# Kernel optimization log

Measured on AMD Instinct MI355X. Metric: run time of the kernel, lower is better.

The kernel has to match this reference:

```python
import jax, jax.numpy as jnp
import numpy as np

DIM = 256
NUM_HEADS = 8
HEAD_DIM = DIM // NUM_HEADS
SCALE = HEAD_DIM ** -0.5


def setup_inputs() -> dict:
    key = jax.random.key(0)
    ks = jax.random.split(key, 8)
    B, C, H, W = 2, DIM, 64, 64
    s = 0.02
    return {
        "dec_feat": jax.random.normal(ks[0], (B, C, H, W), dtype=jnp.float32),
        "enc_feat": jax.random.normal(ks[1], (B, C, H, W), dtype=jnp.float32),
        "Wq": jax.random.normal(ks[2], (C, C), dtype=jnp.float32) * s,
        "bq": jnp.zeros((C,), dtype=jnp.float32),
        "Wkv": jax.random.normal(ks[3], (2 * C, C), dtype=jnp.float32) * s,
        "bkv": jnp.zeros((2 * C,), dtype=jnp.float32),
        "Wo": jax.random.normal(ks[4], (C, C), dtype=jnp.float32) * s,
        "bo": jnp.zeros((C,), dtype=jnp.float32),
    }


def reference(dec_feat, enc_feat, Wq, bq, Wkv, bkv, Wo, bo):
    B, C, H, W = dec_feat.shape
    N = H * W
    hd = HEAD_DIM
    # 1x1 convs == per-pixel linear maps over channels
    q = jnp.einsum('bchw,dc->bdhw', dec_feat, Wq) + bq[None, :, None, None]
    kv = jnp.einsum('bchw,dc->bdhw', enc_feat, Wkv) + bkv[None, :, None, None]
    k, v = jnp.split(kv, 2, axis=1)
    # [B, C, H, W] -> [B, heads, N, head_dim]
    def to_heads(x):
        return x.reshape(B, NUM_HEADS, hd, N).transpose(0, 1, 3, 2)
    qh, kh, vh = to_heads(q), to_heads(k), to_heads(v)
    attn = jnp.einsum('bhnd,bhmd->bhnm', qh, kh) * SCALE  # [B,h,N,N]
    attn = jax.nn.softmax(attn, axis=-1)
    out = jnp.einsum('bhnm,bhmd->bhnd', attn, vh)  # [B,h,N,hd]
    out = out.transpose(0, 1, 3, 2).reshape(B, C, H, W)
    out = jnp.einsum('bchw,dc->bdhw', out, Wo) + bo[None, :, None, None]
    return out
```

## Files before the change

kernel.cpp:

```cpp
#include <hip/hip_runtime.h>
#include <hip/hip_bf16.h>

#define B_ 2
#define C_ 256
#define N_ 4096
#define NH_ 8
#define HD_ 32
#define SCALE_ 0.17677669529663687f
#define LOG2E_ 1.4426950408889634f

typedef __attribute__((ext_vector_type(8))) short bf16x8;
typedef __attribute__((ext_vector_type(4))) float f32x4;

__device__ inline short f2b(float f) {
    __hip_bfloat16 h = __float2bfloat16(f);
    return __builtin_bit_cast(short, h);
}

__device__ inline unsigned pk2(float a, float b) {
    unsigned r;
    asm("v_cvt_pk_bf16_f32 %0, %1, %2" : "=v"(r) : "v"(a), "v"(b));
    return r;
}

__global__ __launch_bounds__(256) void wcvt(
    const float* __restrict__ Wq, const float* __restrict__ Wkv,
    const float* __restrict__ Wo, short* __restrict__ Wall)
{
    const int i = (blockIdx.x * 256 + threadIdx.x) * 8;
    const float* src; int off;
    if (i < 65536)       { src = Wq;  off = i; }
    else if (i < 196608) { src = Wkv; off = i - 65536; }
    else                 { src = Wo;  off = i - 196608; }
    float4 a = ((const float4*)(src + off))[0];
    float4 c = ((const float4*)(src + off))[1];
    uint2 u0, u1;
    u0.x = pk2(a.x, a.y); u0.y = pk2(a.z, a.w);
    u1.x = pk2(c.x, c.y); u1.y = pk2(c.z, c.w);
    *(uint2*)(Wall + i)     = u0;
    *(uint2*)(Wall + i + 4) = u1;
}

__global__ __launch_bounds__(256) void proj_qkv(
    const float* __restrict__ dec, const float* __restrict__ enc,
    const short* __restrict__ Wall, const float* __restrict__ bq,
    const float* __restrict__ bkv,
    short* __restrict__ Qb, short* __restrict__ Kb, short* __restrict__ Vb)
{
    const int b = blockIdx.z, y = blockIdx.y;
    const int n0 = blockIdx.x * 64;
    const float* In   = (y == 0) ? dec : enc;
    const float* bias = (y == 0) ? bq : ((y == 1) ? bkv : bkv + 256);
    const int wbase = y * 256;

    const int tid = threadIdx.x;
    const int w = tid >> 6, l = tid & 63, lg = l >> 4, lr = l & 15;

    __shared__ short eld[8][64][40];

    f32x4 acc[4][4] = {};
    const float* Inb = In + (size_t)b * C_ * N_;

    for (int c0 = 0; c0 < C_; c0 += 32) {
        bf16x8 af[4];
        #pragma unroll
        for (int db = 0; db < 4; db++)
            af[db] = *(const bf16x8*)&Wall[
                (size_t)(wbase + w * 64 + db * 16 + lr) * C_ + c0 + lg * 8];
        #pragma unroll
        for (int nb = 0; nb < 4; nb++) {
            const int n = n0 + nb * 16 + lr;
            const float* ip = Inb + (size_t)(c0 + 8 * lg) * N_ + n;
            float t0 = ip[0],            t1 = ip[(size_t)N_];
            float t2 = ip[2*(size_t)N_], t3 = ip[3*(size_t)N_];
            float t4 = ip[4*(size_t)N_], t5 = ip[5*(size_t)N_];
            float t6 = ip[6*(size_t)N_], t7 = ip[7*(size_t)N_];
            union { bf16x8 v; unsigned u[4]; } bu;
            bu.u[0] = pk2(t0, t1); bu.u[1] = pk2(t2, t3);
            bu.u[2] = pk2(t4, t5); bu.u[3] = pk2(t6, t7);
            #pragma unroll
            for (int db = 0; db < 4; db++)
                acc[db][nb] = __builtin_amdgcn_mfma_f32_16x16x32_bf16(
                    af[db], bu.v, acc[db][nb], 0, 0, 0);
        }
    }

    if (y < 2) {
        const float sA = (y == 0) ? (SCALE_ * LOG2E_) : 1.0f;
        #pragma unroll
        for (int db = 0; db < 4; db++) {
            #pragma unroll
            for (int r = 0; r < 4; r++) {
                const int dloc = w * 64 + db * 16 + lg * 4 + r;
                const float bs = bias[dloc];
                #pragma unroll
                for (int nb = 0; nb < 4; nb++) {
                    const int nloc = nb * 16 + lr;
                    eld[dloc >> 5][nloc][dloc & 31]
                        = f2b((acc[db][nb][r] + bs) * sA);
                }
            }
        }
        __syncthreads();
        const int hh = tid >> 5, j = tid & 31;
        short* dst = ((y == 0) ? Qb : Kb)
            + (((size_t)(b * NH_ + hh) * N_) + n0 + 2 * j) * HD_;
        #pragma unroll
        for (int i = 0; i < 4; i++)
            ((uint4*)dst)[i] = *(const uint4*)&eld[hh][2 * j][i * 8];
        #pragma unroll
        for (int i = 0; i < 4; i++)
            ((uint4*)(dst + HD_))[i] = *(const uint4*)&eld[hh][2 * j + 1][i * 8];
    } else {
        #pragma unroll
        for (int db = 0; db < 4; db++) {
            #pragma unroll
            for (int r = 0; r < 4; r++) {
                const int dloc = w * 64 + db * 16 + lg * 4 + r;
                const float bs = bias[dloc];
                #pragma unroll
                for (int nb = 0; nb < 4; nb++) {
                    const int n = n0 + nb * 16 + lr;
                    Vb[((size_t)(b * C_) + dloc) * N_ + n]
                        = f2b(acc[db][nb][r] + bs);
                }
            }
        }
    }
}

__global__ __launch_bounds__(512) void attn_kernel(
    const short* __restrict__ Qb, const short* __restrict__ Kb,
    const short* __restrict__ Vb, short* __restrict__ AO)
{
    const int lin = blockIdx.x + 32 * (blockIdx.y + 8 * blockIdx.z);
    const int wg  = (lin & 7) * 64 + (lin >> 3);
    const int qblk = wg & 31, h = (wg >> 5) & 7, b = wg >> 8;

    const int tid = threadIdx.x, w = tid >> 6, l = tid & 63;
    const int lg = l >> 4, lr = l & 15;
    const int q0  = qblk * 128 + (w & 3) * 32;
    const int khq = w >> 2;

    const short* Qp = Qb + ((size_t)(b * NH_ + h) * N_) * HD_;
    const short* Kp = Kb + ((size_t)(b * NH_ + h) * N_) * HD_;
    const short* Vp = Vb + ((size_t)(b * NH_ + h) * HD_) * N_;

    __shared__ short Kt[2][2][64][32];
    __shared__ short Vt[2][2][32][64];
    __shared__ float cmb[4][64][20];

    const int sh = tid >> 8;
    const int su = tid & 255;
    const int kkey = su >> 2, kslot = su & 3;
    const int kphys = (kslot ^ ((kkey >> 1) & 3)) * 8;
    const int ksrc = ((kkey >> 4) & 1) * 32 + ((kkey >> 2) & 3) * 8
                   + ((kkey >> 5) & 1) * 4 + (kkey & 3);
    const int vd = su >> 3, vslot = su & 7;
    const int vphys = (vslot ^ (vd & 7)) * 8;

    const int krd = (lg ^ ((lr >> 1) & 3)) * 8;

    bf16x8 qf0 = *(const bf16x8*)&Qp[(size_t)(q0 + lr) * HD_ + lg * 8];
    bf16x8 qf1 = *(const bf16x8*)&Qp[(size_t)(q0 + 16 + lr) * HD_ + lg * 8];

    f32x4 accA0 = {}, accA1 = {}, accB0 = {}, accB1 = {};
    float lsrA[4] = {0, 0, 0, 0}, lsrB[4] = {0, 0, 0, 0};

    const int NT = 2048 / 64;

    if (sh == 0) {
        uint4 p0 = *(const uint4*)(Kp + (size_t)ksrc * HD_ + kslot * 8);
        uint4 p1 = *(const uint4*)(Kp + (size_t)(2048 + ksrc) * HD_ + kslot * 8);
        *(uint4*)&Kt[0][0][kkey][kphys] = p0;
        *(uint4*)&Kt[0][1][kkey][kphys] = p1;
    } else {
        uint4 p0 = *(const uint4*)(Vp + (size_t)vd * N_ + vslot * 8);
        uint4 p1 = *(const uint4*)(Vp + (size_t)vd * N_ + 2048 + vslot * 8);
        *(uint4*)&Vt[0][0][vd][vphys] = p0;
        *(uint4*)&Vt[0][1][vd][vphys] = p1;
    }
    __syncthreads();

    int cur = 0;
    for (int it = 0; it < NT; ++it) {
        uint4 pr0, pr1;
        const int mn = (it + 1) * 64;
        if (it + 1 < NT) {
            if (sh == 0) {
                pr0 = *(const uint4*)(Kp + (size_t)(mn + ksrc) * HD_ + kslot * 8);
                pr1 = *(const uint4*)(Kp + (size_t)(2048 + mn + ksrc) * HD_ + kslot * 8);
            } else {
                pr0 = *(const uint4*)(Vp + (size_t)vd * N_ + mn + vslot * 8);
                pr1 = *(const uint4*)(Vp + (size_t)vd * N_ + 2048 + mn + vslot * 8);
            }
        }

        bf16x8 kf[4];
        #pragma unroll
        for (int t = 0; t < 4; t++)
            kf[t] = *(const bf16x8*)&Kt[cur][khq][16 * t + lr][krd];

        f32x4 z = {};
        f32x4 sA[4], sB[4];
        #pragma unroll
        for (int t = 0; t < 4; t++)
            sA[t] = __builtin_amdgcn_mfma_f32_16x16x32_bf16(kf[t], qf0, z, 0, 0, 0);
        #pragma unroll
        for (int t = 0; t < 4; t++)
            sB[t] = __builtin_amdgcn_mfma_f32_16x16x32_bf16(kf[t], qf1, z, 0, 0, 0);

        bf16x8 vf[2][2];
        #pragma unroll
        for (int c = 0; c < 2; c++)
            #pragma unroll
            for (int hh = 0; hh < 2; hh++)
                vf[c][hh] = *(const bf16x8*)&Vt[cur][khq][16 * hh + lr]
                                [((4 * c + lg) ^ (lr & 7)) * 8];

        float pA[4][4], pB[4][4];
        #pragma unroll
        for (int t = 0; t < 4; t++)
            #pragma unroll
            for (int r = 0; r < 4; r++) {
                pA[t][r] = __builtin_amdgcn_exp2f(sA[t][r]);
                lsrA[r] += pA[t][r];
                pB[t][r] = __builtin_amdgcn_exp2f(sB[t][r]);
                lsrB[r] += pB[t][r];
            }

        #pragma unroll
        for (int c = 0; c < 2; c++) {
            union { bf16x8 v; unsigned u[4]; } pu;
            pu.u[0] = pk2(pA[c][0], pA[c][1]);
            pu.u[1] = pk2(pA[c][2], pA[c][3]);
            pu.u[2] = pk2(pA[c + 2][0], pA[c + 2][1]);
            pu.u[3] = pk2(pA[c + 2][2], pA[c + 2][3]);
            accA0 = __builtin_amdgcn_mfma_f32_16x16x32_bf16(vf[c][0], pu.v, accA0, 0, 0, 0);
            accA1 = __builtin_amdgcn_mfma_f32_16x16x32_bf16(vf[c][1], pu.v, accA1, 0, 0, 0);
        }
        #pragma unroll
        for (int c = 0; c < 2; c++) {
            union { bf16x8 v; unsigned u[4]; } pu;
            pu.u[0] = pk2(pB[c][0], pB[c][1]);
            pu.u[1] = pk2(pB[c][2], pB[c][3]);
            pu.u[2] = pk2(pB[c + 2][0], pB[c + 2][1]);
            pu.u[3] = pk2(pB[c + 2][2], pB[c + 2][3]);
            accB0 = __builtin_amdgcn_mfma_f32_16x16x32_bf16(vf[c][0], pu.v, accB0, 0, 0, 0);
            accB1 = __builtin_amdgcn_mfma_f32_16x16x32_bf16(vf[c][1], pu.v, accB1, 0, 0, 0);
        }

        if (it + 1 < NT) {
            if (sh == 0) {
                *(uint4*)&Kt[cur ^ 1][0][kkey][kphys] = pr0;
                *(uint4*)&Kt[cur ^ 1][1][kkey][kphys] = pr1;
            } else {
                *(uint4*)&Vt[cur ^ 1][0][vd][vphys] = pr0;
                *(uint4*)&Vt[cur ^ 1][1][vd][vphys] = pr1;
            }
        }
        __syncthreads();
        cur ^= 1;
    }

    float lsumA = (lsrA[0] + lsrA[1]) + (lsrA[2] + lsrA[3]);
    float lsumB = (lsrB[0] + lsrB[1]) + (lsrB[2] + lsrB[3]);

    if (w >= 4) {
        float* p = &cmb[w - 4][l][0];
        *(f32x4*)(p + 0)  = accA0;  *(f32x4*)(p + 4)  = accA1;
        *(f32x4*)(p + 8)  = accB0;  *(f32x4*)(p + 12) = accB1;
        p[16] = lsumA; p[17] = lsumB;
    }
    __syncthreads();
    if (w < 4) {
        const float* p = &cmb[w][l][0];
        f32x4 o0 = *(const f32x4*)(p + 0),  o1 = *(const f32x4*)(p + 4);
        f32x4 o2 = *(const f32x4*)(p + 8),  o3 = *(const f32x4*)(p + 12);
        #pragma unroll
        for (int r = 0; r < 4; r++) {
            accA0[r] += o0[r]; accA1[r] += o1[r];
            accB0[r] += o2[r]; accB1[r] += o3[r];
        }
        lsumA += p[16]; lsumB += p[17];

        lsumA += __shfl_xor(lsumA, 16);
        lsumA += __shfl_xor(lsumA, 32);
        lsumB += __shfl_xor(lsumB, 16);
        lsumB += __shfl_xor(lsumB, 32);

        {
            const float inv = 1.0f / lsumA;
            uint2 o;
            o.x = pk2(accA0[0] * inv, accA0[1] * inv);
            o.y = pk2(accA0[2] * inv, accA0[3] * inv);
            *(uint2*)&AO[((size_t)b * N_ + q0 + lr) * C_ + h * HD_ + 4 * lg] = o;
            o.x = pk2(accA1[0] * inv, accA1[1] * inv);
            o.y = pk2(accA1[2] * inv, accA1[3] * inv);
            *(uint2*)&AO[((size_t)b * N_ + q0 + lr) * C_ + h * HD_ + 16 + 4 * lg] = o;
        }
        {
            const float inv = 1.0f / lsumB;
            uint2 o;
            o.x = pk2(accB0[0] * inv, accB0[1] * inv);
            o.y = pk2(accB0[2] * inv, accB0[3] * inv);
            *(uint2*)&AO[((size_t)b * N_ + q0 + 16 + lr) * C_ + h * HD_ + 4 * lg] = o;
            o.x = pk2(accB1[0] * inv, accB1[1] * inv);
            o.y = pk2(accB1[2] * inv, accB1[3] * inv);
            *(uint2*)&AO[((size_t)b * N_ + q0 + 16 + lr) * C_ + h * HD_ + 16 + 4 * lg] = o;
        }
    }
}

__global__ __launch_bounds__(256) void proj_out(
    const short* __restrict__ AO, const short* __restrict__ Wall,
    const float* __restrict__ bias, float* __restrict__ Out)
{
    const int b = blockIdx.z;
    const int n0 = blockIdx.x * 32;
    const int tid = threadIdx.x, w = tid >> 6, l = tid & 63, lg = l >> 4, lr = l & 15;

    f32x4 acc[4][2] = {};

    for (int c0 = 0; c0 < C_; c0 += 32) {
        bf16x8 af[4];
        #pragma unroll
        for (int db = 0; db < 4; db++)
            af[db] = *(const bf16x8*)&Wall[
                (size_t)(768 + w * 64 + db * 16 + lr) * C_ + c0 + lg * 8];
        #pragma unroll
        for (int nb = 0; nb < 2; nb++) {
            bf16x8 bfr = *(const bf16x8*)&AO[
                ((size_t)b * N_ + n0 + nb * 16 + lr) * C_ + c0 + lg * 8];
            #pragma unroll
            for (int db = 0; db < 4; db++)
                acc[db][nb] = __builtin_amdgcn_mfma_f32_16x16x32_bf16(
                    af[db], bfr, acc[db][nb], 0, 0, 0);
        }
    }

    #pragma unroll
    for (int db = 0; db < 4; db++) {
        #pragma unroll
        for (int r = 0; r < 4; r++) {
            const int d = w * 64 + db * 16 + lg * 4 + r;
            const float bs = bias[d];
            #pragma unroll
            for (int nb = 0; nb < 2; nb++)
                Out[((size_t)(b * C_) + d) * N_ + n0 + nb * 16 + lr]
                    = acc[db][nb][r] + bs;
        }
    }
}

extern "C" void kernel_launch(void* const* d_in, const int* in_sizes, int n_in,
                              void* d_out, int out_size, void* d_ws, size_t ws_size,
                              hipStream_t stream) {
    const float* dec = (const float*)d_in[0];
    const float* enc = (const float*)d_in[1];
    const float* Wq  = (const float*)d_in[2];
    const float* bq  = (const float*)d_in[3];
    const float* Wkv = (const float*)d_in[4];
    const float* bkv = (const float*)d_in[5];
    const float* Wo  = (const float*)d_in[6];
    const float* bo  = (const float*)d_in[7];
    float* out = (float*)d_out;

    const size_t SEG = (size_t)B_ * N_ * C_;
    short* Qb   = (short*)d_ws;
    short* Kb   = Qb + SEG;
    short* Vb   = Kb + SEG;
    short* AOb  = Vb + SEG;
    short* Wall = AOb + SEG;

    wcvt<<<128, 256, 0, stream>>>(Wq, Wkv, Wo, Wall);
    proj_qkv<<<dim3(N_ / 64, 3, B_), 256, 0, stream>>>(dec, enc, Wall, bq, bkv,
                                                       Qb, Kb, Vb);
    attn_kernel<<<dim3(N_ / 128, NH_, B_), 512, 0, stream>>>(Qb, Kb, Vb, AOb);
    proj_out<<<dim3(N_ / 32, 1, B_), 256, 0, stream>>>(AOb, Wall, bo, out);
}
```

Before: 86.10 us.

## Load K and V fragments directly from global memory, dropping LDS staging

Removes the double-buffered LDS tiles for K and V along with the per-iteration __syncthreads. Each wave now reads its MFMA K and V fragments straight from global memory, relying on L1/L2 caching because the four waves sharing a key half reuse the same data. Launch bounds are raised to request 4 blocks per CU for higher occupancy. The trade-off is more global/cache traffic and exposed load latency with no software prefetch, in exchange for no barriers and less LDS use.

New measurement: 129.0 us. +49.9%, slower.

```diff
diff --git a/kernel.cpp b/kernel.cpp
--- a/kernel.cpp
+++ b/kernel.cpp
@@ -129,7 +129,7 @@
     }
 }
 
-__global__ __launch_bounds__(512) void attn_kernel(
+__global__ __launch_bounds__(512, 4) void attn_kernel(
     const short* __restrict__ Qb, const short* __restrict__ Kb,
     const short* __restrict__ Vb, short* __restrict__ AO)
 {
@@ -146,20 +146,9 @@
     const short* Kp = Kb + ((size_t)(b * NH_ + h) * N_) * HD_;
     const short* Vp = Vb + ((size_t)(b * NH_ + h) * HD_) * N_;
 
-    __shared__ short Kt[2][2][64][32];
-    __shared__ short Vt[2][2][32][64];
     __shared__ float cmb[4][64][20];
 
-    const int sh = tid >> 8;
-    const int su = tid & 255;
-    const int kkey = su >> 2, kslot = su & 3;
-    const int kphys = (kslot ^ ((kkey >> 1) & 3)) * 8;
-    const int ksrc = ((kkey >> 4) & 1) * 32 + ((kkey >> 2) & 3) * 8
-                   + ((kkey >> 5) & 1) * 4 + (kkey & 3);
-    const int vd = su >> 3, vslot = su & 7;
-    const int vphys = (vslot ^ (vd & 7)) * 8;
-
-    const int krd = (lg ^ ((lr >> 1) & 3)) * 8;
+    const int krow = 8 * (lr >> 2) + (lr & 3);
 
     bf16x8 qf0 = *(const bf16x8*)&Qp[(size_t)(q0 + lr) * HD_ + lg * 8];
     bf16x8 qf1 = *(const bf16x8*)&Qp[(size_t)(q0 + 16 + lr) * HD_ + lg * 8];
@@ -167,39 +156,16 @@
     f32x4 accA0 = {}, accA1 = {}, accB0 = {}, accB1 = {};
     float lsrA[4] = {0, 0, 0, 0}, lsrB[4] = {0, 0, 0, 0};
 
-    const int NT = 2048 / 64;
-
-    if (sh == 0) {
-        uint4 p0 = *(const uint4*)(Kp + (size_t)ksrc * HD_ + kslot * 8);
-        uint4 p1 = *(const uint4*)(Kp + (size_t)(2048 + ksrc) * HD_ + kslot * 8);
-        *(uint4*)&Kt[0][0][kkey][kphys] = p0;
-        *(uint4*)&Kt[0][1][kkey][kphys] = p1;
-    } else {
-        uint4 p0 = *(const uint4*)(Vp + (size_t)vd * N_ + vslot * 8);
-        uint4 p1 = *(const uint4*)(Vp + (size_t)vd * N_ + 2048 + vslot * 8);
-        *(uint4*)&Vt[0][0][vd][vphys] = p0;
-        *(uint4*)&Vt[0][1][vd][vphys] = p1;
-    }
-    __syncthreads();
-
-    int cur = 0;
-    for (int it = 0; it < NT; ++it) {
-        uint4 pr0, pr1;
-        const int mn = (it + 1) * 64;
-        if (it + 1 < NT) {
-            if (sh == 0) {
-                pr0 = *(const uint4*)(Kp + (size_t)(mn + ksrc) * HD_ + kslot * 8);
-                pr1 = *(const uint4*)(Kp + (size_t)(2048 + mn + ksrc) * HD_ + kslot * 8);
-            } else {
-                pr0 = *(const uint4*)(Vp + (size_t)vd * N_ + mn + vslot * 8);
-                pr1 = *(const uint4*)(Vp + (size_t)vd * N_ + 2048 + mn + vslot * 8);
-            }
-        }
+    const int base = khq * 2048;
+
+    for (int it = 0; it < 32; ++it) {
+        const int m0 = base + it * 64;
 
         bf16x8 kf[4];
         #pragma unroll
         for (int t = 0; t < 4; t++)
-            kf[t] = *(const bf16x8*)&Kt[cur][khq][16 * t + lr][krd];
+            kf[t] = *(const bf16x8*)&Kp[
+                (size_t)(m0 + 32 * (t & 1) + 4 * (t >> 1) + krow) * HD_ + lg * 8];
 
         f32x4 z = {};
         f32x4 sA[4], sB[4];
@@ -215,8 +181,8 @@
         for (int c = 0; c < 2; c++)
             #pragma unroll
             for (int hh = 0; hh < 2; hh++)
-                vf[c][hh] = *(const bf16x8*)&Vt[cur][khq][16 * hh + lr]
-                                [((4 * c + lg) ^ (lr & 7)) * 8];
+                vf[c][hh] = *(const bf16x8*)&Vp[
+                    (size_t)(16 * hh + lr) * N_ + m0 + 32 * c + 8 * lg];
 
         float pA[4][4], pB[4][4];
         #pragma unroll
@@ -249,18 +215,6 @@
             accB0 = __builtin_amdgcn_mfma_f32_16x16x32_bf16(vf[c][0], pu.v, accB0, 0, 0, 0);
             accB1 = __builtin_amdgcn_mfma_f32_16x16x32_bf16(vf[c][1], pu.v, accB1, 0, 0, 0);
         }
-
-        if (it + 1 < NT) {
-            if (sh == 0) {
-                *(uint4*)&Kt[cur ^ 1][0][kkey][kphys] = pr0;
-                *(uint4*)&Kt[cur ^ 1][1][kkey][kphys] = pr1;
-            } else {
-                *(uint4*)&Vt[cur ^ 1][0][vd][vphys] = pr0;
-                *(uint4*)&Vt[cur ^ 1][1][vd][vphys] = pr1;
-            }
-        }
-        __syncthreads();
-        cur ^= 1;
     }
 
     float lsumA = (lsrA[0] + lsrA[1]) + (lsrA[2] + lsrA[3]);
```
